# Kernel tuning notes

Hardware: AMD Instinct MI355X
Metric: run time of the kernel (lower is better)

## Reference

```python
import jax, jax.numpy as jnp
import numpy as np

N_BLADES = 8
D_BLADE = 128
D_FFN = 512
LN_EPS = 1e-5


def _build_cayley_signs():
    """Cl(3,0) Cayley table: blades indexed by bitmask over {e1,e2,e3}.
    signs[i, j, k] = s where blade_i * blade_j = s * blade_k (Euclidean metric)."""
    def reorder_sign(a, b):
        a >>= 1
        total = 0
        while a:
            total += bin(a & b).count('1')
            a >>= 1
        return 1.0 if total % 2 == 0 else -1.0
    signs = np.zeros((8, 8, 8), dtype=np.float32)
    for i in range(8):
        for j in range(8):
            signs[i, j, i ^ j] = reorder_sign(i, j)
    return jnp.asarray(signs)


def setup_inputs() -> dict:
    key = jax.random.key(0)
    k_x, k_g, k_u, k_d = jax.random.split(key, 4)
    B, T = 4, 4096
    x = jax.random.normal(k_x, (B, T, N_BLADES, D_BLADE), dtype=jnp.float32)
    return {
        'x': x,
        'interaction_weights': jnp.full((N_BLADES, N_BLADES), 0.1, dtype=jnp.float32),
        'geo_gate': jnp.asarray(0.5, dtype=jnp.float32),
        'ln_w': jnp.ones((D_BLADE,), dtype=jnp.float32),
        'ln_b': jnp.zeros((D_BLADE,), dtype=jnp.float32),
        'w_gate': jax.random.normal(k_g, (D_FFN, D_BLADE), dtype=jnp.float32) * 0.02,
        'w_up': jax.random.normal(k_u, (D_FFN, D_BLADE), dtype=jnp.float32) * 0.02,
        'w_down': jax.random.normal(k_d, (D_BLADE, D_FFN), dtype=jnp.float32) * 0.02,
        'cayley_signs': _build_cayley_signs(),
    }


def reference(x, interaction_weights, geo_gate, ln_w, ln_b, w_gate, w_up, w_down, cayley_signs):
    # --- full geometric self-product via Cayley table ---
    w = jax.nn.sigmoid(interaction_weights)              # (i, j)
    signed = cayley_signs * w[:, :, None]                # (i, j, k): fold weights into sign tensor
    # result[b,t,k,d] = sum_ij signed[i,j,k] * x[b,t,i,d] * x[b,t,j,d]
    geo = jnp.einsum('btid,btjd,ijk->btkd', x, x, signed)
    # --- residual gate between geometric product and input ---
    gate = jax.nn.sigmoid(geo_gate)
    mixed = gate * geo + (1.0 - gate) * x                # (B, T, N, D)
    # --- per-blade LayerNorm over d_blade ---
    mu = jnp.mean(mixed, axis=-1, keepdims=True)
    var = jnp.mean(jnp.square(mixed - mu), axis=-1, keepdims=True)
    normed = (mixed - mu) * jax.lax.rsqrt(var + LN_EPS) * ln_w + ln_b
    # --- SwiGLU FFN (no biases) ---
    g = jnp.einsum('btnd,fd->btnf', normed, w_gate)
    u = jnp.einsum('btnd,fd->btnf', normed, w_up)
    h = jax.nn.silu(g) * u
    out = jnp.einsum('btnf,df->btnd', h, w_down)
    return x + out
```

## Files before the change

### kernel.cpp

```cpp
#include <hip/hip_runtime.h>
#include <hip/hip_bf16.h>

typedef unsigned short ushort_t;
typedef __bf16 bf16_t;
typedef bf16_t bf16x8 __attribute__((ext_vector_type(8)));
typedef unsigned short u16x8v __attribute__((ext_vector_type(8)));
typedef float f32x4 __attribute__((ext_vector_type(4)));
typedef unsigned uint32x2 __attribute__((ext_vector_type(2)));
typedef unsigned uint32x4 __attribute__((ext_vector_type(4)));

#define D 128
#define NB 8
#define DFFN 512
#define LN_EPS 1e-5f

#define BARRIER_LGKM() asm volatile("s_waitcnt lgkmcnt(0)\n\ts_barrier" ::: "memory")
#define PIN(v) asm volatile("" : "+v"(v))

__device__ __forceinline__ ushort_t bf16_rne(float f) {
  union { float f; unsigned u; } c; c.f = f;
  unsigned u = c.u;
  unsigned r = (u + 0x7FFFu + ((u >> 16) & 1u)) >> 16;
  return (ushort_t)r;
}

__device__ __forceinline__ unsigned cvt_pk_bf16(float lo, float hi) {
  unsigned r;
  asm("v_cvt_pk_bf16_f32 %0, %1, %2" : "=v"(r) : "v"(lo), "v"(hi));
  return r;
}

__device__ __forceinline__ bf16x8 loadfrag_bf(const ushort_t* p) {
  u16x8v v = *(const u16x8v*)p;
  return __builtin_bit_cast(bf16x8, v);
}

__device__ __forceinline__ bf16x8 load8_cvt(const float* p) {
  f32x4 a = *(const f32x4*)p;
  f32x4 b = *(const f32x4*)(p + 4);
  u16x8v r;
  r[0] = bf16_rne(a[0]); r[1] = bf16_rne(a[1]);
  r[2] = bf16_rne(a[2]); r[3] = bf16_rne(a[3]);
  r[4] = bf16_rne(b[0]); r[5] = bf16_rne(b[1]);
  r[6] = bf16_rne(b[2]); r[7] = bf16_rne(b[3]);
  return __builtin_bit_cast(bf16x8, r);
}

__device__ __forceinline__ f32x4 mfma16(bf16x8 a, bf16x8 b, f32x4 c) {
  return __builtin_amdgcn_mfma_f32_16x16x32_bf16(a, b, c, 0, 0, 0);
}

__device__ __forceinline__ float readlane_f(float v, int lane) {
  return __builtin_bit_cast(float, __builtin_amdgcn_readlane(__builtin_bit_cast(int, v), lane));
}

__device__ __forceinline__ float fast_rcp(float x) {
  return __builtin_amdgcn_rcpf(x);
}

__global__ void cvt_weights(const float* __restrict__ wg,
                            const float* __restrict__ wu,
                            const float* __restrict__ wd,
                            ushort_t* __restrict__ o) {
  int i = blockIdx.x * 256 + threadIdx.x;
  const int n1 = DFFN * D;
  float v;
  if (i < n1)            v = wg[i];
  else if (i < 2 * n1)   v = wu[i - n1];
  else                   v = wd[i - 2 * n1];
  o[i] = bf16_rne(v);
}

__global__ __launch_bounds__(256, 3)
void geo_ffn_fused(const float* __restrict__ x,
                   const float* __restrict__ iw,
                   const float* __restrict__ geo_gate,
                   const float* __restrict__ ln_w,
                   const float* __restrict__ ln_b,
                   const float* __restrict__ cayley,
                   const ushort_t* __restrict__ wg_bf,
                   const ushort_t* __restrict__ wu_bf,
                   const ushort_t* __restrict__ wd_bf,
                   float* __restrict__ out) {
  __shared__ ushort_t A[64 * 128];
  __shared__ ushort_t Hb[2][64 * 64];

  const int tid = threadIdx.x;
  const int w = tid >> 6;
  const int l = tid & 63;
  const int lg = l >> 4;
  const int ln16 = l & 15;

  const long tok0 = (long)blockIdx.x * 8;
  const long row0 = tok0 * NB;

  bf16x8 bg[4], bu[4], bd[2][2];
  {
    const int frow = w * 16 + ln16;
#pragma unroll
    for (int ks = 0; ks < 4; ++ks) {
      bg[ks] = loadfrag_bf(wg_bf + frow * D + ks * 32 + lg * 8);
      bu[ks] = loadfrag_bf(wu_bf + frow * D + ks * 32 + lg * 8);
    }
#pragma unroll
    for (int nt = 0; nt < 2; ++nt) {
      int dcol = w * 32 + nt * 16 + ln16;
#pragma unroll
      for (int k2 = 0; k2 < 2; ++k2)
        bd[nt][k2] = loadfrag_bf(wd_bf + dcol * DFFN + k2 * 32 + lg * 8);
    }
  }

  float cd[8], cp[28];
  {
    float sgv;
    int i_l = l >> 3, j_l = l & 7;
    float s = cayley[(i_l * 8 + j_l) * 8 + (i_l ^ j_l)];
    sgv = s / (1.0f + __expf(-iw[i_l * 8 + j_l]));
#pragma unroll
    for (int i = 0; i < 8; ++i) cd[i] = readlane_f(sgv, i * 8 + i);
    int p = 0;
#pragma unroll
    for (int i = 0; i < 8; ++i)
#pragma unroll
      for (int j = i + 1; j < 8; ++j) { cp[p] = readlane_f(sgv, i * 8 + j) + readlane_f(sgv, j * 8 + i); ++p; }
  }
  const float gate = 1.0f / (1.0f + __expf(-geo_gate[0]));
  const float ogate = 1.0f - gate;
  const float2 lw = *(const float2*)(ln_w + 2 * l);
  const float2 lb = *(const float2*)(ln_b + 2 * l);

  for (int tt = 0; tt < 2; ++tt) {
    const int ltok = w * 2 + tt;
    const float* xp = x + (tok0 + ltok) * (long)(NB * D);
    float2 xv[8];
#pragma unroll
    for (int i = 0; i < 8; ++i) xv[i] = *(const float2*)(xp + i * D + 2 * l);
    float2 geo[8];
#pragma unroll
    for (int k = 0; k < 8; ++k) { geo[k].x = 0.f; geo[k].y = 0.f; }
#pragma unroll
    for (int i = 0; i < 8; ++i) {
      geo[0].x += cd[i] * xv[i].x * xv[i].x;
      geo[0].y += cd[i] * xv[i].y * xv[i].y;
    }
    {
      int p = 0;
#pragma unroll
      for (int i = 0; i < 8; ++i)
#pragma unroll
        for (int j = i + 1; j < 8; ++j) {
          int k = i ^ j;
          geo[k].x += cp[p] * (xv[i].x * xv[j].x);
          geo[k].y += cp[p] * (xv[i].y * xv[j].y);
          ++p;
        }
    }
#pragma unroll
    for (int k = 0; k < 8; ++k) {
      float mx = gate * geo[k].x + ogate * xv[k].x;
      float my = gate * geo[k].y + ogate * xv[k].y;
      float s1 = mx + my;
      float s2 = mx * mx + my * my;
#pragma unroll
      for (int off = 32; off; off >>= 1) {
        s1 += __shfl_xor(s1, off, 64);
        s2 += __shfl_xor(s2, off, 64);
      }
      float mu = s1 * (1.0f / 128.0f);
      float rs = rsqrtf(s2 * (1.0f / 128.0f) - mu * mu + LN_EPS);
      float nx = (mx - mu) * rs * lw.x + lb.x;
      float ny = (my - mu) * rs * lw.y + lb.y;
      int row = ltok * 8 + k;
      int colb = (4 * l) ^ ((row & 7) << 4);
      *(unsigned*)((char*)A + row * 256 + colb) = cvt_pk_bf16(nx, ny);
    }
  }

  BARRIER_LGKM();

  bf16x8 afr[4][4];
#pragma unroll
  for (int mt = 0; mt < 4; ++mt) {
    const int row = mt * 16 + ln16;
#pragma unroll
    for (int ks = 0; ks < 4; ++ks) {
      int unit = (ks * 4 + lg) ^ (row & 7);
      afr[mt][ks] = *(const bf16x8*)&A[row * 128 + unit * 8];
    }
  }
#pragma unroll
  for (int mt = 0; mt < 4; ++mt)
#pragma unroll
    for (int ks = 0; ks < 4; ++ks)
      PIN(afr[mt][ks]);

  f32x4 oacc[4][2];
#pragma unroll
  for (int mt = 0; mt < 4; ++mt)
#pragma unroll
    for (int nt = 0; nt < 2; ++nt)
#pragma unroll
      for (int r = 0; r < 4; ++r) oacc[mt][nt][r] = 0.f;

#pragma unroll
  for (int ch = 0; ch < 8; ++ch) {
    ushort_t* Hc = &Hb[ch & 1][0];

#pragma unroll
    for (int mt = 0; mt < 4; ++mt) {
      const int row = mt * 16 + ln16;
      f32x4 gacc = 0.f, uacc = 0.f;
      __builtin_amdgcn_s_setprio(1);
#pragma unroll
      for (int ks = 0; ks < 4; ++ks) {
        gacc = mfma16(bg[ks], afr[mt][ks], gacc);
        uacc = mfma16(bu[ks], afr[mt][ks], uacc);
      }
      __builtin_amdgcn_s_setprio(0);
      float h[4];
#pragma unroll
      for (int r = 0; r < 4; ++r) {
        float gv = gacc[r];
        h[r] = gv * fast_rcp(1.0f + __expf(-gv)) * uacc[r];
      }
      uint32x2 pk;
      pk[0] = cvt_pk_bf16(h[0], h[1]);
      pk[1] = cvt_pk_bf16(h[2], h[3]);
      int u = (w * 2 + (lg >> 1)) ^ (row & 7);
      *(uint32x2*)((char*)Hc + row * 128 + u * 16 + (lg & 1) * 8) = pk;
    }

    if (ch < 7) {
      const int frow = (ch + 1) * 64 + w * 16 + ln16;
#pragma unroll
      for (int ks = 0; ks < 4; ++ks) {
        bg[ks] = loadfrag_bf(wg_bf + frow * D + ks * 32 + lg * 8);
        bu[ks] = loadfrag_bf(wu_bf + frow * D + ks * 32 + lg * 8);
      }
    }

    BARRIER_LGKM();

    __builtin_amdgcn_s_setprio(1);
#pragma unroll
    for (int mt = 0; mt < 4; ++mt) {
      const int m = mt * 16 + ln16;
#pragma unroll
      for (int k2 = 0; k2 < 2; ++k2) {
        int u = (k2 * 4 + lg) ^ (m & 7);
        bf16x8 hf = *(const bf16x8*)((const char*)Hc + m * 128 + u * 16);
        oacc[mt][0] = mfma16(hf, bd[0][k2], oacc[mt][0]);
        oacc[mt][1] = mfma16(hf, bd[1][k2], oacc[mt][1]);
      }
    }
    __builtin_amdgcn_s_setprio(0);

    if (ch < 7) {
#pragma unroll
      for (int nt = 0; nt < 2; ++nt) {
        int dcol = w * 32 + nt * 16 + ln16;
#pragma unroll
        for (int k2 = 0; k2 < 2; ++k2)
          bd[nt][k2] = loadfrag_bf(wd_bf + dcol * DFFN + (ch + 1) * 64 + k2 * 32 + lg * 8);
      }
    }
  }

#pragma unroll
  for (int mt = 0; mt < 4; ++mt) {
#pragma unroll
    for (int r = 0; r < 4; ++r) {
      long rowg = row0 + mt * 16 + lg * 4 + r;
      const float* xp = x + rowg * D;
      float* op = out + rowg * D;
#pragma unroll
      for (int nt = 0; nt < 2; ++nt) {
        int d = w * 32 + nt * 16 + ln16;
        op[d] = xp[d] + oacc[mt][nt][r];
      }
    }
  }
}

__global__ __launch_bounds__(256, 2)
void fused_geo_ffn_f32w(const float* __restrict__ x,
                        const float* __restrict__ iw,
                        const float* __restrict__ geo_gate,
                        const float* __restrict__ ln_w,
                        const float* __restrict__ ln_b,
                        const float* __restrict__ w_gate_f,
                        const float* __restrict__ w_up_f,
                        const float* __restrict__ w_down_f,
                        const float* __restrict__ cayley,
                        float* __restrict__ out) {
  __shared__ float sg[64];
  __shared__ ushort_t A_lds[128 * 128];
  __shared__ ushort_t H_lds[128 * 64];

  const int tid = threadIdx.x;
  const int w = tid >> 6;
  const int l = tid & 63;
  const int lg = l >> 4;
  const int ln16 = l & 15;
  const int kbase = lg * 8;

  if (tid < 64) {
    int i = tid >> 3, j = tid & 7;
    float s = cayley[(i * 8 + j) * 8 + (i ^ j)];
    sg[tid] = s / (1.0f + __expf(-iw[i * 8 + j]));
  }
  __syncthreads();
  float sgr[64];
#pragma unroll
  for (int t = 0; t < 64; ++t) sgr[t] = sg[t];

  const float gate = 1.0f / (1.0f + __expf(-geo_gate[0]));
  const float2 lw = *(const float2*)(ln_w + 2 * l);
  const float2 lb = *(const float2*)(ln_b + 2 * l);
  const long tok0 = (long)blockIdx.x * 16;

  for (int tt = 0; tt < 4; ++tt) {
    int ltok = w * 4 + tt;
    const float* xp = x + (tok0 + ltok) * (long)(NB * D);
    float2 xv[8];
#pragma unroll
    for (int i = 0; i < 8; ++i) xv[i] = *(const float2*)(xp + i * D + 2 * l);
#pragma unroll
    for (int k = 0; k < 8; ++k) {
      float2 g; g.x = 0.f; g.y = 0.f;
#pragma unroll
      for (int i = 0; i < 8; ++i) {
        float s = sgr[i * 8 + (i ^ k)];
        g.x += s * xv[i].x * xv[i ^ k].x;
        g.y += s * xv[i].y * xv[i ^ k].y;
      }
      float2 m;
      m.x = gate * g.x + (1.0f - gate) * xv[k].x;
      m.y = gate * g.y + (1.0f - gate) * xv[k].y;
      float s1 = m.x + m.y;
      float s2 = m.x * m.x + m.y * m.y;
#pragma unroll
      for (int off = 32; off; off >>= 1) {
        s1 += __shfl_xor(s1, off, 64);
        s2 += __shfl_xor(s2, off, 64);
      }
      float mu = s1 * (1.0f / 128.0f);
      float rs = rsqrtf(s2 * (1.0f / 128.0f) - mu * mu + LN_EPS);
      float nx = (m.x - mu) * rs * lw.x + lb.x;
      float ny = (m.y - mu) * rs * lw.y + lb.y;
      int row = ltok * 8 + k;
      int colb = (4 * l) ^ ((row & 7) << 4);
      *(unsigned*)((char*)A_lds + row * 256 + colb) = cvt_pk_bf16(nx, ny);
    }
  }
  __syncthreads();

  f32x4 oacc[8][2];
#pragma unroll
  for (int mt = 0; mt < 8; ++mt)
#pragma unroll
    for (int nt = 0; nt < 2; ++nt)
#pragma unroll
      for (int r = 0; r < 4; ++r) oacc[mt][nt][r] = 0.f;

  for (int ch = 0; ch < 8; ++ch) {
    const int fbase = ch * 64 + w * 16 + ln16;
    bf16x8 bg[4], bu[4];
#pragma unroll
    for (int ks = 0; ks < 4; ++ks) {
      int koff = ks * 32 + kbase;
      bg[ks] = load8_cvt(w_gate_f + fbase * D + koff);
      bu[ks] = load8_cvt(w_up_f + fbase * D + koff);
    }
#pragma unroll
    for (int mt = 0; mt < 8; ++mt) {
      const int row = mt * 16 + ln16;
      f32x4 gacc = 0.f, uacc = 0.f;
#pragma unroll
      for (int ks = 0; ks < 4; ++ks) {
        int colb = ((ks * 32 + kbase) * 2) ^ ((row & 7) << 4);
        bf16x8 a = *(const bf16x8*)((const char*)A_lds + row * 256 + colb);
        gacc = mfma16(bg[ks], a, gacc);
        uacc = mfma16(bu[ks], a, uacc);
      }
      float h[4];
#pragma unroll
      for (int r = 0; r < 4; ++r) {
        float gv = gacc[r], uv = uacc[r];
        h[r] = gv * __builtin_amdgcn_rcpf(1.0f + __expf(-gv)) * uv;
      }
      uint32x2 pk;
      pk[0] = cvt_pk_bf16(h[0], h[1]);
      pk[1] = cvt_pk_bf16(h[2], h[3]);
      int u = (w * 2 + (lg >> 1)) ^ (row & 7);
      *(uint32x2*)&H_lds[row * 64 + u * 8 + (lg & 1) * 4] = pk;
    }
    __syncthreads();
#pragma unroll
    for (int mt = 0; mt < 8; ++mt) {
      const int row = mt * 16 + ln16;
#pragma unroll
      for (int ks = 0; ks < 2; ++ks) {
        int u = (ks * 4 + lg) ^ (row & 7);
        bf16x8 hfrag = *(const bf16x8*)&H_lds[row * 64 + u * 8];
        int dcol0 = w * 32 + ln16;
        int foff = ch * 64 + ks * 32 + kbase;
        bf16x8 b0 = load8_cvt(w_down_f + dcol0 * DFFN + foff);
        bf16x8 b1 = load8_cvt(w_down_f + (dcol0 + 16) * DFFN + foff);
        oacc[mt][0] = mfma16(hfrag, b0, oacc[mt][0]);
        oacc[mt][1] = mfma16(hfrag, b1, oacc[mt][1]);
      }
    }
    __syncthreads();
  }

  const long rowg0 = tok0 * NB;
#pragma unroll
  for (int mt = 0; mt < 8; ++mt) {
#pragma unroll
    for (int r = 0; r < 4; ++r) {
      long row = rowg0 + mt * 16 + lg * 4 + r;
      const float* xp = x + row * D;
      float* op = out + row * D;
#pragma unroll
      for (int nt = 0; nt < 2; ++nt) {
        int d = w * 32 + nt * 16 + ln16;
        op[d] = xp[d] + oacc[mt][nt][r];
      }
    }
  }
}

extern "C" void kernel_launch(void* const* d_in, const int* in_sizes, int n_in,
                              void* d_out, int out_size, void* d_ws, size_t ws_size,
                              hipStream_t stream) {
  const float* x   = (const float*)d_in[0];
  const float* iw  = (const float*)d_in[1];
  const float* gg  = (const float*)d_in[2];
  const float* lnw = (const float*)d_in[3];
  const float* lnb = (const float*)d_in[4];
  const float* wg  = (const float*)d_in[5];
  const float* wu  = (const float*)d_in[6];
  const float* wd  = (const float*)d_in[7];
  const float* cs  = (const float*)d_in[8];
  float* out = (float*)d_out;

  const int ntok = in_sizes[0] / (NB * D);
  const int wtot = 3 * DFFN * D;
  const size_t wbytes = (size_t)wtot * 2;

  if (ws_size >= wbytes) {
    ushort_t* wbf = (ushort_t*)d_ws;
    cvt_weights<<<wtot / 256, 256, 0, stream>>>(wg, wu, wd, wbf);
    geo_ffn_fused<<<ntok / 8, 256, 0, stream>>>(
        x, iw, gg, lnw, lnb, cs,
        wbf, wbf + DFFN * D, wbf + 2 * DFFN * D, out);
  } else {
    fused_geo_ffn_f32w<<<ntok / 16, 256, 0, stream>>>(
        x, iw, gg, lnw, lnb, wg, wu, wd, cs, out);
  }
}
```

Before: 113.7 us.

## Double block to 16 tokens with 8 waves and stream A fragments from LDS

```diff
diff --git a/kernel.cpp b/kernel.cpp
--- a/kernel.cpp
+++ b/kernel.cpp
@@ -15,7 +15,6 @@
 #define LN_EPS 1e-5f
 
 #define BARRIER_LGKM() asm volatile("s_waitcnt lgkmcnt(0)\n\ts_barrier" ::: "memory")
-#define PIN(v) asm volatile("" : "+v"(v))
 
 __device__ __forceinline__ ushort_t bf16_rne(float f) {
   union { float f; unsigned u; } c; c.f = f;
@@ -71,7 +70,7 @@
   o[i] = bf16_rne(v);
 }
 
-__global__ __launch_bounds__(256, 3)
+__global__ __launch_bounds__(512, 2)
 void geo_ffn_fused(const float* __restrict__ x,
                    const float* __restrict__ iw,
                    const float* __restrict__ geo_gate,
@@ -82,21 +81,23 @@
                    const ushort_t* __restrict__ wu_bf,
                    const ushort_t* __restrict__ wd_bf,
                    float* __restrict__ out) {
-  __shared__ ushort_t A[64 * 128];
-  __shared__ ushort_t Hb[2][64 * 64];
+  __shared__ ushort_t A[128 * 128];
+  __shared__ ushort_t Hb[2][128 * 64];
 
   const int tid = threadIdx.x;
   const int w = tid >> 6;
   const int l = tid & 63;
   const int lg = l >> 4;
   const int ln16 = l & 15;
-
-  const long tok0 = (long)blockIdx.x * 8;
+  const int mh = w >> 2;
+  const int fs = w & 3;
+
+  const long tok0 = (long)blockIdx.x * 16;
   const long row0 = tok0 * NB;
 
   bf16x8 bg[4], bu[4], bd[2][2];
   {
-    const int frow = w * 16 + ln16;
+    const int frow = fs * 16 + ln16;
 #pragma unroll
     for (int ks = 0; ks < 4; ++ks) {
       bg[ks] = loadfrag_bf(wg_bf + frow * D + ks * 32 + lg * 8);
@@ -104,7 +105,7 @@
     }
 #pragma unroll
     for (int nt = 0; nt < 2; ++nt) {
-      int dcol = w * 32 + nt * 16 + ln16;
+      int dcol = fs * 32 + nt * 16 + ln16;
 #pragma unroll
       for (int k2 = 0; k2 < 2; ++k2)
         bd[nt][k2] = loadfrag_bf(wd_bf + dcol * DFFN + k2 * 32 + lg * 8);
@@ -179,22 +180,6 @@
 
   BARRIER_LGKM();
 
-  bf16x8 afr[4][4];
-#pragma unroll
-  for (int mt = 0; mt < 4; ++mt) {
-    const int row = mt * 16 + ln16;
-#pragma unroll
-    for (int ks = 0; ks < 4; ++ks) {
-      int unit = (ks * 4 + lg) ^ (row & 7);
-      afr[mt][ks] = *(const bf16x8*)&A[row * 128 + unit * 8];
-    }
-  }
-#pragma unroll
-  for (int mt = 0; mt < 4; ++mt)
-#pragma unroll
-    for (int ks = 0; ks < 4; ++ks)
-      PIN(afr[mt][ks]);
-
   f32x4 oacc[4][2];
 #pragma unroll
   for (int mt = 0; mt < 4; ++mt)
@@ -209,13 +194,15 @@
 
 #pragma unroll
     for (int mt = 0; mt < 4; ++mt) {
-      const int row = mt * 16 + ln16;
+      const int row = mh * 64 + mt * 16 + ln16;
       f32x4 gacc = 0.f, uacc = 0.f;
       __builtin_amdgcn_s_setprio(1);
 #pragma unroll
       for (int ks = 0; ks < 4; ++ks) {
-        gacc = mfma16(bg[ks], afr[mt][ks], gacc);
-        uacc = mfma16(bu[ks], afr[mt][ks], uacc);
+        int unit = (ks * 4 + lg) ^ (row & 7);
+        bf16x8 a = *(const bf16x8*)&A[row * 128 + unit * 8];
+        gacc = mfma16(bg[ks], a, gacc);
+        uacc = mfma16(bu[ks], a, uacc);
       }
       __builtin_amdgcn_s_setprio(0);
       float h[4];
@@ -227,12 +214,12 @@
       uint32x2 pk;
       pk[0] = cvt_pk_bf16(h[0], h[1]);
       pk[1] = cvt_pk_bf16(h[2], h[3]);
-      int u = (w * 2 + (lg >> 1)) ^ (row & 7);
+      int u = (fs * 2 + (lg >> 1)) ^ (row & 7);
       *(uint32x2*)((char*)Hc + row * 128 + u * 16 + (lg & 1) * 8) = pk;
     }
 
     if (ch < 7) {
-      const int frow = (ch + 1) * 64 + w * 16 + ln16;
+      const int frow = (ch + 1) * 64 + fs * 16 + ln16;
 #pragma unroll
       for (int ks = 0; ks < 4; ++ks) {
         bg[ks] = loadfrag_bf(wg_bf + frow * D + ks * 32 + lg * 8);
@@ -245,7 +232,7 @@
     __builtin_amdgcn_s_setprio(1);
 #pragma unroll
     for (int mt = 0; mt < 4; ++mt) {
-      const int m = mt * 16 + ln16;
+      const int m = mh * 64 + mt * 16 + ln16;
 #pragma unroll
       for (int k2 = 0; k2 < 2; ++k2) {
         int u = (k2 * 4 + lg) ^ (m & 7);
@@ -259,7 +246,7 @@
     if (ch < 7) {
 #pragma unroll
       for (int nt = 0; nt < 2; ++nt) {
-        int dcol = w * 32 + nt * 16 + ln16;
+        int dcol = fs * 32 + nt * 16 + ln16;
 #pragma unroll
         for (int k2 = 0; k2 < 2; ++k2)
           bd[nt][k2] = loadfrag_bf(wd_bf + dcol * DFFN + (ch + 1) * 64 + k2 * 32 + lg * 8);
@@ -271,12 +258,12 @@
   for (int mt = 0; mt < 4; ++mt) {
 #pragma unroll
     for (int r = 0; r < 4; ++r) {
-      long rowg = row0 + mt * 16 + lg * 4 + r;
+      long rowg = row0 + mh * 64 + mt * 16 + lg * 4 + r;
       const float* xp = x + rowg * D;
       float* op = out + rowg * D;
 #pragma unroll
       for (int nt = 0; nt < 2; ++nt) {
-        int d = w * 32 + nt * 16 + ln16;
+        int d = fs * 32 + nt * 16 + ln16;
         op[d] = xp[d] + oacc[mt][nt][r];
       }
     }
@@ -453,7 +440,7 @@
   if (ws_size >= wbytes) {
     ushort_t* wbf = (ushort_t*)d_ws;
     cvt_weights<<<wtot / 256, 256, 0, stream>>>(wg, wu, wd, wbf);
-    geo_ffn_fused<<<ntok / 8, 256, 0, stream>>>(
+    geo_ffn_fused<<<ntok / 16, 512, 0, stream>>>(
         x, iw, gg, lnw, lnb, cs,
         wbf, wbf + DFFN * D, wbf + 2 * DFFN * D, out);
   } else {
```

Result: slower. 136.2 us (+19.8%).

## Software-pipeline gate/up GEMM of next chunk with down-proj of current chunk

Applied to the files above, without the earlier changes.

```diff
diff --git a/kernel.cpp b/kernel.cpp
--- a/kernel.cpp
+++ b/kernel.cpp
@@ -204,41 +204,40 @@
       for (int r = 0; r < 4; ++r) oacc[mt][nt][r] = 0.f;
 
 #pragma unroll
+  for (int mt = 0; mt < 4; ++mt) {
+    const int row = mt * 16 + ln16;
+    f32x4 gacc = 0.f, uacc = 0.f;
+#pragma unroll
+    for (int ks = 0; ks < 4; ++ks) {
+      gacc = mfma16(bg[ks], afr[mt][ks], gacc);
+      uacc = mfma16(bu[ks], afr[mt][ks], uacc);
+    }
+    float h[4];
+#pragma unroll
+    for (int r = 0; r < 4; ++r) {
+      float gv = gacc[r];
+      h[r] = gv * fast_rcp(1.0f + __expf(-gv)) * uacc[r];
+    }
+    uint32x2 pk;
+    pk[0] = cvt_pk_bf16(h[0], h[1]);
+    pk[1] = cvt_pk_bf16(h[2], h[3]);
+    int u = (w * 2 + (lg >> 1)) ^ (row & 7);
+    *(uint32x2*)((char*)&Hb[0][0] + row * 128 + u * 16 + (lg & 1) * 8) = pk;
+  }
+
+  {
+    const int frow = 64 + w * 16 + ln16;
+#pragma unroll
+    for (int ks = 0; ks < 4; ++ks) {
+      bg[ks] = loadfrag_bf(wg_bf + frow * D + ks * 32 + lg * 8);
+      bu[ks] = loadfrag_bf(wu_bf + frow * D + ks * 32 + lg * 8);
+    }
+  }
+
+#pragma unroll
   for (int ch = 0; ch < 8; ++ch) {
     ushort_t* Hc = &Hb[ch & 1][0];
-
-#pragma unroll
-    for (int mt = 0; mt < 4; ++mt) {
-      const int row = mt * 16 + ln16;
-      f32x4 gacc = 0.f, uacc = 0.f;
-      __builtin_amdgcn_s_setprio(1);
-#pragma unroll
-      for (int ks = 0; ks < 4; ++ks) {
-        gacc = mfma16(bg[ks], afr[mt][ks], gacc);
-        uacc = mfma16(bu[ks], afr[mt][ks], uacc);
-      }
-      __builtin_amdgcn_s_setprio(0);
-      float h[4];
-#pragma unroll
-      for (int r = 0; r < 4; ++r) {
-        float gv = gacc[r];
-        h[r] = gv * fast_rcp(1.0f + __expf(-gv)) * uacc[r];
-      }
-      uint32x2 pk;
-      pk[0] = cvt_pk_bf16(h[0], h[1]);
-      pk[1] = cvt_pk_bf16(h[2], h[3]);
-      int u = (w * 2 + (lg >> 1)) ^ (row & 7);
-      *(uint32x2*)((char*)Hc + row * 128 + u * 16 + (lg & 1) * 8) = pk;
-    }
-
-    if (ch < 7) {
-      const int frow = (ch + 1) * 64 + w * 16 + ln16;
-#pragma unroll
-      for (int ks = 0; ks < 4; ++ks) {
-        bg[ks] = loadfrag_bf(wg_bf + frow * D + ks * 32 + lg * 8);
-        bu[ks] = loadfrag_bf(wu_bf + frow * D + ks * 32 + lg * 8);
-      }
-    }
+    ushort_t* Hn = &Hb[(ch + 1) & 1][0];
 
     BARRIER_LGKM();
 
@@ -246,6 +245,7 @@
 #pragma unroll
     for (int mt = 0; mt < 4; ++mt) {
       const int m = mt * 16 + ln16;
+
 #pragma unroll
       for (int k2 = 0; k2 < 2; ++k2) {
         int u = (k2 * 4 + lg) ^ (m & 7);
@@ -253,6 +253,26 @@
         oacc[mt][0] = mfma16(hf, bd[0][k2], oacc[mt][0]);
         oacc[mt][1] = mfma16(hf, bd[1][k2], oacc[mt][1]);
       }
+
+      if (ch < 7) {
+        f32x4 gacc = 0.f, uacc = 0.f;
+#pragma unroll
+        for (int ks = 0; ks < 4; ++ks) {
+          gacc = mfma16(bg[ks], afr[mt][ks], gacc);
+          uacc = mfma16(bu[ks], afr[mt][ks], uacc);
+        }
+        float h[4];
+#pragma unroll
+        for (int r = 0; r < 4; ++r) {
+          float gv = gacc[r];
+          h[r] = gv * fast_rcp(1.0f + __expf(-gv)) * uacc[r];
+        }
+        uint32x2 pk;
+        pk[0] = cvt_pk_bf16(h[0], h[1]);
+        pk[1] = cvt_pk_bf16(h[2], h[3]);
+        int u = (w * 2 + (lg >> 1)) ^ (m & 7);
+        *(uint32x2*)((char*)Hn + m * 128 + u * 16 + (lg & 1) * 8) = pk;
+      }
     }
     __builtin_amdgcn_s_setprio(0);
 
@@ -263,6 +283,14 @@
 #pragma unroll
         for (int k2 = 0; k2 < 2; ++k2)
           bd[nt][k2] = loadfrag_bf(wd_bf + dcol * DFFN + (ch + 1) * 64 + k2 * 32 + lg * 8);
+      }
+      if (ch < 6) {
+        const int frow = (ch + 2) * 64 + w * 16 + ln16;
+#pragma unroll
+        for (int ks = 0; ks < 4; ++ks) {
+          bg[ks] = loadfrag_bf(wg_bf + frow * D + ks * 32 + lg * 8);
+          bu[ks] = loadfrag_bf(wu_bf + frow * D + ks * 32 + lg * 8);
+        }
       }
     }
   }
```

New measurement: 151.4 us. +33.2%, slower.
